# Optimization experiments

Hardware: AMD Instinct MI355X
Metric: run time of the kernel (lower is better)

The kernel has to match this reference:

```python
import jax, jax.numpy as jnp
import numpy as np
from jax import lax

B, T, D, K = 2, 4096, 128, 256


def setup_inputs() -> dict:
    key = jax.random.key(0)
    ks = jax.random.split(key, 5)
    s = 0.05
    return {
        "z": jax.random.normal(ks[0], (B, T, D), jnp.float32),
        "conv_kernel": jax.random.normal(ks[1], (K, 1, D), jnp.float32) * s,  # flax WIO depthwise
        "conv_bias": jnp.zeros((D,), jnp.float32),
        "Wq": jax.random.normal(ks[2], (D, D), jnp.float32) * s,
        "bq": jnp.zeros((D,), jnp.float32),
        "Wk": jax.random.normal(ks[3], (D, D), jnp.float32) * s,
        "bk": jnp.zeros((D,), jnp.float32),
        "Wo": jax.random.normal(ks[4], (D, D), jnp.float32) * s,
        "bo": jnp.zeros((D,), jnp.float32),
    }


def _sphere_norm(x):
    return x / jnp.maximum(jnp.linalg.norm(x, axis=-1, keepdims=True), 1e-8)


def reference(z, conv_kernel, conv_bias, Wq, bq, Wk, bk, Wo, bo):
    Bv, Tv, Dv = z.shape
    Kv = conv_kernel.shape[0]

    # Depthwise causal memory conv (flax nn.Conv, padding='CAUSAL', groups=D)
    memory_force = lax.conv_general_dilated(
        z, conv_kernel, window_strides=(1,), padding=[(Kv - 1, 0)],
        dimension_numbers=("NWC", "WIO", "NWC"), feature_group_count=Dv,
    ) + conv_bias

    # Keys are computed from the base point z once, shared across RK4 stages
    k_hat = _sphere_norm(z @ Wk + bk)  # [B,T,D]
    mask = jnp.tril(jnp.ones((Tv, Tv), z.dtype))  # causal mask

    def vector_field(z_curr):
        q_hat = _sphere_norm(z_curr @ Wq + bq)
        dots = jnp.einsum("btd,bsd->bts", q_hat, k_hat)  # [B,T,T]
        attn = jnp.sin(dots) * mask  # Kuramoto-style sin coupling, causal
        kuramoto = jnp.einsum("bts,bsd->btd", attn, k_hat) @ Wo + bo
        total = memory_force + kuramoto
        # project to tangent space of the sphere at z_curr
        return total - jnp.sum(total * z_curr, axis=-1, keepdims=True) * z_curr

    h = 1.0

    def retract(z_base, v):
        return _sphere_norm(z_base + v)

    k1 = vector_field(z)
    k2 = vector_field(retract(z, 0.5 * h * k1))
    k3 = vector_field(retract(z, 0.5 * h * k2))
    k4 = vector_field(retract(z, h * k3))
    v_final = (h / 6.0) * (k1 + 2 * k2 + 2 * k3 + k4)
    return retract(z, v_final)
```

## Files before the change

kernel.cpp:

```cpp
#include <hip/hip_runtime.h>
#include <hip/hip_bf16.h>

#define BB 2
#define TT 4096
#define DD 128
#define KK 256
#define NROW (BB*TT)
#define NELT (NROW*DD)

typedef _Float16 f16;
typedef __attribute__((ext_vector_type(8))) f16 half8;
typedef __attribute__((ext_vector_type(4))) float f32x4;

__global__ __launch_bounds__(256) void k_proj(
    const float* __restrict__ z, const float* __restrict__ Wk, const float* __restrict__ bk,
    f16* __restrict__ khb, f16* __restrict__ khT)
{
  __shared__ float Ws[DD*DD];
  __shared__ float zs[32*DD];
  int tid = threadIdx.x;
  int r0 = blockIdx.x * 32;
  #pragma unroll
  for (int it = 0; it < 16; it++){
    int idx = tid + it*256;
    *(f32x4*)(Ws + idx*4) = *(const f32x4*)(Wk + (size_t)idx*4);
  }
  #pragma unroll
  for (int it = 0; it < 4; it++){
    int idx = tid + it*256;
    *(f32x4*)(zs + idx*4) = *(const f32x4*)(z + (size_t)r0*DD + idx*4);
  }
  __syncthreads();
  int c = tid & 15, rr = tid >> 4;
  float acc0[8], acc1[8];
  #pragma unroll
  for (int u = 0; u < 8; u++){ float bv = bk[c*8+u]; acc0[u] = bv; acc1[u] = bv; }
  const float* zr0 = zs + rr*DD;
  const float* zr1 = zs + (rr+16)*DD;
  #pragma unroll 4
  for (int i = 0; i < DD; i++){
    f32x4 w0 = *(const f32x4*)(Ws + i*DD + c*8);
    f32x4 w1 = *(const f32x4*)(Ws + i*DD + c*8 + 4);
    float a0 = zr0[i], a1 = zr1[i];
    #pragma unroll
    for (int u = 0; u < 4; u++){
      acc0[u]   = fmaf(a0, w0[u], acc0[u]);   acc1[u]   = fmaf(a1, w0[u], acc1[u]);
      acc0[4+u] = fmaf(a0, w1[u], acc0[4+u]); acc1[4+u] = fmaf(a1, w1[u], acc1[4+u]);
    }
  }
  float s0 = 0.f, s1 = 0.f;
  #pragma unroll
  for (int u = 0; u < 8; u++){ s0 = fmaf(acc0[u], acc0[u], s0); s1 = fmaf(acc1[u], acc1[u], s1); }
  #pragma unroll
  for (int m = 1; m < 16; m <<= 1){ s0 += __shfl_xor(s0, m, 16); s1 += __shfl_xor(s1, m, 16); }
  float inv0 = 1.f / fmaxf(sqrtf(s0), 1e-8f);
  float inv1 = 1.f / fmaxf(sqrtf(s1), 1e-8f);
  half8 h0, h1;
  #pragma unroll
  for (int u = 0; u < 8; u++){ h0[u] = (f16)(acc0[u]*inv0); h1[u] = (f16)(acc1[u]*inv1); }
  int row0 = r0 + rr, row1 = row0 + 16;
  *(half8*)(khb + (size_t)row0*DD + c*8) = h0;
  *(half8*)(khb + (size_t)row1*DD + c*8) = h1;
  int b = row0 >> 12, t0 = row0 & 4095, t1 = row1 & 4095;
  #pragma unroll
  for (int u = 0; u < 8; u++){
    khT[((size_t)b*DD + c*8 + u)*TT + t0] = h0[u];
    khT[((size_t)b*DD + c*8 + u)*TT + t1] = h1[u];
  }
}

__global__ __launch_bounds__(256) void k_conv(
    const float* __restrict__ z, const float* __restrict__ ck, const float* __restrict__ cb,
    float* __restrict__ mf)
{
  int tid = threadIdx.x;
  int d = tid & 127, tg = tid >> 7;
  int bid = blockIdx.x;
  int b = bid >> 8;
  int tbase = ((bid & 255) << 4) + tg*8;
  const float* zb = z + (size_t)b*TT*DD;
  float acc[8];
  #pragma unroll
  for (int j = 0; j < 8; j++) acc[j] = 0.f;
  float ckq[8];
  #pragma unroll
  for (int u = 0; u < 8; u++) ckq[u] = 0.f;
  int sstart = tbase - (KK-1);
  for (int ch = 0; ch < 33; ch++){
    #pragma unroll
    for (int u = 0; u < 8; u++){
      int base = ch*8 + u;
      int s = sstart + base;
      float zv = ((unsigned)s < (unsigned)TT && base < 263) ? zb[(size_t)s*DD + d] : 0.f;
      ckq[u] = (base < KK) ? ck[(size_t)base*DD + d] : 0.f;
      #pragma unroll
      for (int j = 0; j < 8; j++) acc[j] = fmaf(ckq[(u-j)&7], zv, acc[j]);
    }
  }
  float cbv = cb[d];
  #pragma unroll
  for (int j = 0; j < 8; j++)
    mf[((size_t)b*TT + tbase + j)*DD + d] = acc[j] + cbv;
}

__global__ __launch_bounds__(256) void k_q(
    const float* __restrict__ zcur, const float* __restrict__ Wq, const float* __restrict__ bq,
    f16* __restrict__ qhb)
{
  __shared__ float Ws[DD*DD];
  __shared__ float zs[32*DD];
  int tid = threadIdx.x;
  int r0 = blockIdx.x * 32;
  #pragma unroll
  for (int it = 0; it < 16; it++){
    int idx = tid + it*256;
    *(f32x4*)(Ws + idx*4) = *(const f32x4*)(Wq + (size_t)idx*4);
  }
  #pragma unroll
  for (int it = 0; it < 4; it++){
    int idx = tid + it*256;
    *(f32x4*)(zs + idx*4) = *(const f32x4*)(zcur + (size_t)r0*DD + idx*4);
  }
  __syncthreads();
  int c = tid & 15, rr = tid >> 4;
  float acc0[8], acc1[8];
  #pragma unroll
  for (int u = 0; u < 8; u++){ float bv = bq[c*8+u]; acc0[u] = bv; acc1[u] = bv; }
  const float* zr0 = zs + rr*DD;
  const float* zr1 = zs + (rr+16)*DD;
  #pragma unroll 4
  for (int i = 0; i < DD; i++){
    f32x4 w0 = *(const f32x4*)(Ws + i*DD + c*8);
    f32x4 w1 = *(const f32x4*)(Ws + i*DD + c*8 + 4);
    float a0 = zr0[i], a1 = zr1[i];
    #pragma unroll
    for (int u = 0; u < 4; u++){
      acc0[u]   = fmaf(a0, w0[u], acc0[u]);   acc1[u]   = fmaf(a1, w0[u], acc1[u]);
      acc0[4+u] = fmaf(a0, w1[u], acc0[4+u]); acc1[4+u] = fmaf(a1, w1[u], acc1[4+u]);
    }
  }
  float s0 = 0.f, s1 = 0.f;
  #pragma unroll
  for (int u = 0; u < 8; u++){ s0 = fmaf(acc0[u], acc0[u], s0); s1 = fmaf(acc1[u], acc1[u], s1); }
  #pragma unroll
  for (int m = 1; m < 16; m <<= 1){ s0 += __shfl_xor(s0, m, 16); s1 += __shfl_xor(s1, m, 16); }
  float inv0 = 1.f / fmaxf(sqrtf(s0), 1e-8f);
  float inv1 = 1.f / fmaxf(sqrtf(s1), 1e-8f);
  half8 h0, h1;
  #pragma unroll
  for (int u = 0; u < 8; u++){ h0[u] = (f16)(acc0[u]*inv0); h1[u] = (f16)(acc1[u]*inv1); }
  *(half8*)(qhb + (size_t)(r0+rr)*DD + c*8) = h0;
  *(half8*)(qhb + (size_t)(r0+rr+16)*DD + c*8) = h1;
}

#define QTILE 128
#define NQT3 (TT/QTILE)
#define NCHUNK 272

__global__ __launch_bounds__(256,2) void k_attn4(
    const f16* __restrict__ qhb, const f16* __restrict__ khb,
    const f16* __restrict__ khT, float* __restrict__ part)
{
  int bid = blockIdx.x;
  int b = bid / NCHUNK;
  int rem = bid - b*NCHUNK;
  int qt = 0, chunk = 0;
  #pragma unroll 1
  for (int j = 0; j < NQT3; j++){
    int nch = (j + 2) >> 1;
    if (rem < nch){ qt = j; chunk = rem; break; }
    rem -= nch;
  }
  int kt0 = chunk * 4;
  int kt1 = min(kt0 + 3, 2*qt + 1);
  int t0 = qt * QTILE;

  __shared__ __align__(16) f16 Kb[64*136];
  __shared__ __align__(16) f16 Kt[128*72];
  __shared__ __align__(16) float Ps[4][32*68];

  int tid  = threadIdx.x;
  int w    = tid >> 6;
  int lane = tid & 63;
  int n16  = lane & 15;
  int g    = lane >> 4;

  const f16* qg  = qhb + (size_t)b*TT*DD;
  const f16* kg  = khb + (size_t)b*TT*DD;
  const f16* ktg = khT + (size_t)b*DD*TT;

  int sb_r  = tid >> 4, sb_c = (tid & 15)*8;
  int st_r  = tid >> 3, st_c = (tid & 7)*8;

  half8 qa[2][4];
  #pragma unroll
  for (int p = 0; p < 2; p++){
    const f16* qrow = qg + (size_t)(t0 + 32*w + 16*p + n16)*DD + g*8;
    #pragma unroll
    for (int c = 0; c < 4; c++) qa[p][c] = *(const half8*)(qrow + 32*c);
  }
  f32x4 acc[2][8];
  #pragma unroll
  for (int p = 0; p < 2; p++)
    #pragma unroll
    for (int i = 0; i < 8; i++) acc[p][i] = (f32x4){0.f,0.f,0.f,0.f};

  float* psw = &Ps[w][0];

  half8 sKb[4], sKt[4];
  {
    int s0 = kt0 * 64;
    #pragma unroll
    for (int it = 0; it < 4; it++)
      sKb[it] = *(const half8*)(kg + (size_t)(s0 + sb_r + it*16)*DD + sb_c);
    #pragma unroll
    for (int it = 0; it < 4; it++)
      sKt[it] = *(const half8*)(ktg + (size_t)(st_r + it*32)*TT + s0 + st_c);
  }

  for (int kt = kt0; kt <= kt1; kt++){
    #pragma unroll
    for (int it = 0; it < 4; it++)
      *(half8*)(Kb + (sb_r + it*16)*136 + sb_c) = sKb[it];
    #pragma unroll
    for (int it = 0; it < 4; it++)
      *(half8*)(Kt + (st_r + it*32)*72 + st_c) = sKt[it];
    __syncthreads();

    if (kt < kt1){
      int s0n = (kt+1) * 64;
      #pragma unroll
      for (int it = 0; it < 4; it++)
        sKb[it] = *(const half8*)(kg + (size_t)(s0n + sb_r + it*16)*DD + sb_c);
      #pragma unroll
      for (int it = 0; it < 4; it++)
        sKt[it] = *(const half8*)(ktg + (size_t)(st_r + it*32)*TT + s0n + st_c);
    }

    int s0 = kt * 64;
    f32x4 s_acc[2][4];
    #pragma unroll
    for (int p = 0; p < 2; p++)
      #pragma unroll
      for (int n = 0; n < 4; n++) s_acc[p][n] = (f32x4){0.f,0.f,0.f,0.f};
    #pragma unroll
    for (int c = 0; c < 4; c++){
      #pragma unroll
      for (int n = 0; n < 4; n++){
        half8 bf = *(const half8*)(Kb + (16*n + n16)*136 + 32*c + g*8);
        s_acc[0][n] = __builtin_amdgcn_mfma_f32_16x16x32_f16(qa[0][c], bf, s_acc[0][n], 0,0,0);
        s_acc[1][n] = __builtin_amdgcn_mfma_f32_16x16x32_f16(qa[1][c], bf, s_acc[1][n], 0,0,0);
      }
    }
    #pragma unroll
    for (int p = 0; p < 2; p++){
      int qrow = t0 + 32*w + 16*p + 4*g;
      #pragma unroll
      for (int n = 0; n < 4; n++){
        int key = s0 + 16*n + n16;
        #pragma unroll
        for (int r = 0; r < 4; r++){
          float v = (key <= qrow + r) ? __sinf(s_acc[p][n][r]) : 0.f;
          psw[(16*p + 4*g + r)*68 + 16*n + n16] = v;
        }
      }
    }
    __syncthreads();

    #pragma unroll
    for (int h = 0; h < 2; h++){
      half8 pa[2];
      #pragma unroll
      for (int p = 0; p < 2; p++){
        f32x4 p0 = *(const f32x4*)(psw + (16*p + n16)*68 + 32*h + 8*g);
        f32x4 p1 = *(const f32x4*)(psw + (16*p + n16)*68 + 32*h + 8*g + 4);
        pa[p][0]=(f16)p0[0]; pa[p][1]=(f16)p0[1]; pa[p][2]=(f16)p0[2]; pa[p][3]=(f16)p0[3];
        pa[p][4]=(f16)p1[0]; pa[p][5]=(f16)p1[1]; pa[p][6]=(f16)p1[2]; pa[p][7]=(f16)p1[3];
      }
      #pragma unroll
      for (int nt = 0; nt < 8; nt++){
        half8 bf = *(const half8*)(Kt + (16*nt + n16)*72 + 32*h + 8*g);
        acc[0][nt] = __builtin_amdgcn_mfma_f32_16x16x32_f16(pa[0], bf, acc[0][nt], 0,0,0);
        acc[1][nt] = __builtin_amdgcn_mfma_f32_16x16x32_f16(pa[1], bf, acc[1][nt], 0,0,0);
      }
    }
    __syncthreads();
  }

  float* pb = part + (size_t)bid*(QTILE*DD) + (32*w)*DD;
  #pragma unroll
  for (int p = 0; p < 2; p++){
    #pragma unroll
    for (int nt = 0; nt < 8; nt++){
      #pragma unroll
      for (int r = 0; r < 4; r++){
        pb[(size_t)(16*p + 4*g + r)*DD + 16*nt + n16] = acc[p][nt][r];
      }
    }
  }
}

__global__ __launch_bounds__(256) void k_reduce(
    const float* __restrict__ part, float* __restrict__ att)
{
  int bid = blockIdx.x;
  int rg = bid & 7;
  int qt = (bid >> 3) & 31;
  int b  = bid >> 8;
  int nc = (qt + 2) >> 1;
  int base = ((qt + 1)*(qt + 1)) >> 2;
  int tid = threadIdx.x;
  size_t off = (size_t)rg*(16*DD) + tid*8;
  const float* src = part + ((size_t)b*NCHUNK + base)*(QTILE*DD) + off;
  f32x4 a0 = *(const f32x4*)(src);
  f32x4 a1 = *(const f32x4*)(src + 4);
  for (int c = 1; c < nc; c++){
    const float* s2 = src + (size_t)c*(QTILE*DD);
    f32x4 b0 = *(const f32x4*)(s2);
    f32x4 b1 = *(const f32x4*)(s2 + 4);
    #pragma unroll
    for (int u = 0; u < 4; u++){ a0[u] += b0[u]; a1[u] += b1[u]; }
  }
  float* dst = att + ((size_t)b*TT + (size_t)qt*QTILE)*DD + off;
  *(f32x4*)(dst) = a0;
  *(f32x4*)(dst + 4) = a1;
}

__global__ __launch_bounds__(256) void k_comb(
    const float* __restrict__ z, const float* __restrict__ Wo, const float* __restrict__ bo,
    const float* __restrict__ mf, const float* __restrict__ att,
    const float* __restrict__ zin, float* __restrict__ zout,
    float* __restrict__ vsum, float* __restrict__ out,
    float wsum, float cretr, int first, int last)
{
  __shared__ float Ws[DD*DD];
  __shared__ float As[32*DD];
  int tid = threadIdx.x;
  int r0 = blockIdx.x * 32;
  #pragma unroll
  for (int it = 0; it < 16; it++){
    int idx = tid + it*256;
    *(f32x4*)(Ws + idx*4) = *(const f32x4*)(Wo + (size_t)idx*4);
  }
  #pragma unroll
  for (int it = 0; it < 4; it++){
    int idx = tid + it*256;
    *(f32x4*)(As + idx*4) = *(const f32x4*)(att + (size_t)r0*DD + idx*4);
  }
  __syncthreads();
  int c = tid & 15, rr = tid >> 4;
  float kur0[8], kur1[8];
  #pragma unroll
  for (int u = 0; u < 8; u++){ float bv = bo[c*8+u]; kur0[u] = bv; kur1[u] = bv; }
  const float* ar0 = As + rr*DD;
  const float* ar1 = As + (rr+16)*DD;
  #pragma unroll 4
  for (int i = 0; i < DD; i++){
    f32x4 w0 = *(const f32x4*)(Ws + i*DD + c*8);
    f32x4 w1 = *(const f32x4*)(Ws + i*DD + c*8 + 4);
    float a0 = ar0[i], a1 = ar1[i];
    #pragma unroll
    for (int u = 0; u < 4; u++){
      kur0[u]   = fmaf(a0, w0[u], kur0[u]);   kur1[u]   = fmaf(a1, w0[u], kur1[u]);
      kur0[4+u] = fmaf(a0, w1[u], kur0[4+u]); kur1[4+u] = fmaf(a1, w1[u], kur1[4+u]);
    }
  }
  size_t o0 = (size_t)(r0+rr)*DD + c*8;
  size_t o1 = (size_t)(r0+rr+16)*DD + c*8;
  float tot0[8], tot1[8], zi0[8], zi1[8];
  {
    f32x4 m0a = *(const f32x4*)(mf + o0), m0b = *(const f32x4*)(mf + o0 + 4);
    f32x4 m1a = *(const f32x4*)(mf + o1), m1b = *(const f32x4*)(mf + o1 + 4);
    f32x4 z0a = *(const f32x4*)(zin + o0), z0b = *(const f32x4*)(zin + o0 + 4);
    f32x4 z1a = *(const f32x4*)(zin + o1), z1b = *(const f32x4*)(zin + o1 + 4);
    #pragma unroll
    for (int u = 0; u < 4; u++){
      tot0[u] = m0a[u] + kur0[u]; tot0[4+u] = m0b[u] + kur0[4+u];
      tot1[u] = m1a[u] + kur1[u]; tot1[4+u] = m1b[u] + kur1[4+u];
      zi0[u] = z0a[u]; zi0[4+u] = z0b[u];
      zi1[u] = z1a[u]; zi1[4+u] = z1b[u];
    }
  }
  float p0 = 0.f, p1 = 0.f;
  #pragma unroll
  for (int u = 0; u < 8; u++){ p0 = fmaf(tot0[u], zi0[u], p0); p1 = fmaf(tot1[u], zi1[u], p1); }
  #pragma unroll
  for (int m = 1; m < 16; m <<= 1){ p0 += __shfl_xor(p0, m, 16); p1 += __shfl_xor(p1, m, 16); }
  float ki0[8], ki1[8], vs0[8], vs1[8];
  #pragma unroll
  for (int u = 0; u < 8; u++){
    ki0[u] = tot0[u] - p0 * zi0[u];
    ki1[u] = tot1[u] - p1 * zi1[u];
  }
  if (first){
    #pragma unroll
    for (int u = 0; u < 8; u++){ vs0[u] = wsum*ki0[u]; vs1[u] = wsum*ki1[u]; }
  } else {
    f32x4 v0a = *(const f32x4*)(vsum + o0), v0b = *(const f32x4*)(vsum + o0 + 4);
    f32x4 v1a = *(const f32x4*)(vsum + o1), v1b = *(const f32x4*)(vsum + o1 + 4);
    #pragma unroll
    for (int u = 0; u < 4; u++){
      vs0[u] = fmaf(wsum, ki0[u], v0a[u]); vs0[4+u] = fmaf(wsum, ki0[4+u], v0b[u]);
      vs1[u] = fmaf(wsum, ki1[u], v1a[u]); vs1[4+u] = fmaf(wsum, ki1[4+u], v1b[u]);
    }
  }
  if (!last){
    f32x4 va = {vs0[0],vs0[1],vs0[2],vs0[3]}, vb = {vs0[4],vs0[5],vs0[6],vs0[7]};
    f32x4 vc = {vs1[0],vs1[1],vs1[2],vs1[3]}, vd = {vs1[4],vs1[5],vs1[6],vs1[7]};
    *(f32x4*)(vsum + o0) = va; *(f32x4*)(vsum + o0 + 4) = vb;
    *(f32x4*)(vsum + o1) = vc; *(f32x4*)(vsum + o1 + 4) = vd;
  }
  float nz0[8], nz1[8];
  {
    f32x4 z0a = *(const f32x4*)(z + o0), z0b = *(const f32x4*)(z + o0 + 4);
    f32x4 z1a = *(const f32x4*)(z + o1), z1b = *(const f32x4*)(z + o1 + 4);
    #pragma unroll
    for (int u = 0; u < 4; u++){
      float d0a = last ? vs0[u]*(1.f/6.f)   : cretr*ki0[u];
      float d0b = last ? vs0[4+u]*(1.f/6.f) : cretr*ki0[4+u];
      float d1a = last ? vs1[u]*(1.f/6.f)   : cretr*ki1[u];
      float d1b = last ? vs1[4+u]*(1.f/6.f) : cretr*ki1[4+u];
      nz0[u] = z0a[u] + d0a; nz0[4+u] = z0b[u] + d0b;
      nz1[u] = z1a[u] + d1a; nz1[4+u] = z1b[u] + d1b;
    }
  }
  float n0 = 0.f, n1 = 0.f;
  #pragma unroll
  for (int u = 0; u < 8; u++){ n0 = fmaf(nz0[u], nz0[u], n0); n1 = fmaf(nz1[u], nz1[u], n1); }
  #pragma unroll
  for (int m = 1; m < 16; m <<= 1){ n0 += __shfl_xor(n0, m, 16); n1 += __shfl_xor(n1, m, 16); }
  float i0 = 1.f / fmaxf(sqrtf(n0), 1e-8f);
  float i1 = 1.f / fmaxf(sqrtf(n1), 1e-8f);
  float* dst = last ? out : zout;
  f32x4 ra = {nz0[0]*i0, nz0[1]*i0, nz0[2]*i0, nz0[3]*i0};
  f32x4 rb = {nz0[4]*i0, nz0[5]*i0, nz0[6]*i0, nz0[7]*i0};
  f32x4 rc = {nz1[0]*i1, nz1[1]*i1, nz1[2]*i1, nz1[3]*i1};
  f32x4 rd = {nz1[4]*i1, nz1[5]*i1, nz1[6]*i1, nz1[7]*i1};
  *(f32x4*)(dst + o0) = ra; *(f32x4*)(dst + o0 + 4) = rb;
  *(f32x4*)(dst + o1) = rc; *(f32x4*)(dst + o1 + 4) = rd;
}

extern "C" void kernel_launch(void* const* d_in, const int* in_sizes, int n_in,
                              void* d_out, int out_size, void* d_ws, size_t ws_size,
                              hipStream_t stream) {
  const float* z  = (const float*)d_in[0];
  const float* ck = (const float*)d_in[1];
  const float* cb = (const float*)d_in[2];
  const float* Wq = (const float*)d_in[3];
  const float* bq = (const float*)d_in[4];
  const float* Wk = (const float*)d_in[5];
  const float* bk = (const float*)d_in[6];
  const float* Wo = (const float*)d_in[7];
  const float* bo = (const float*)d_in[8];
  float* out = (float*)d_out;

  float* mf   = (float*)d_ws;
  float* zc   = mf   + NELT;
  float* att  = zc   + NELT;
  float* vsum = att  + NELT;
  f16*   khb  = (f16*)(vsum + NELT);
  f16*   khT  = khb  + NELT;
  f16*   qhb  = khT  + NELT;
  float* part = (float*)(qhb + NELT);

  k_proj<<<NROW/32, 256, 0, stream>>>(z, Wk, bk, khb, khT);
  k_conv<<<BB*TT/16, 256, 0, stream>>>(z, ck, cb, mf);

  const float wv[4] = {1.f, 2.f, 2.f, 1.f};
  const float cv[4] = {0.5f, 0.5f, 1.f, 0.f};
  for (int st = 0; st < 4; st++){
    const float* zcur = (st == 0) ? z : zc;
    k_q     <<<NROW/32, 256, 0, stream>>>(zcur, Wq, bq, qhb);
    k_attn4 <<<BB*NCHUNK, 256, 0, stream>>>(qhb, khb, khT, part);
    k_reduce<<<BB*NQT3*8, 256, 0, stream>>>(part, att);
    k_comb  <<<NROW/32, 256, 0, stream>>>(z, Wo, bo, mf, att, zcur, zc, vsum, out,
                                          wv[st], cv[st], st == 0, st == 3);
  }
}
```

Baseline: 316.0 us.

## Store sin scores as fp16, drop redundant barrier, fuse partial reduce into combine

The attention kernel now writes the masked sin scores into a per-wave fp16 LDS buffer instead of fp32. The P-operand load becomes one half8 read with no conversion, LDS use is smaller, and the occupancy hint goes from 2 to 3 blocks. The __syncthreads between score write and read is removed, since each wave only touches its own Ps slice. The separate k_reduce kernel is gone: k_comb sums the chunk partials directly while loading its activation tile, which saves a launch and a round-trip through the att buffer per stage, in exchange for more serial loads inside k_comb.

```diff
diff --git a/kernel.cpp b/kernel.cpp
--- a/kernel.cpp
+++ b/kernel.cpp
@@ -157,7 +157,7 @@
 #define NQT3 (TT/QTILE)
 #define NCHUNK 272
 
-__global__ __launch_bounds__(256,2) void k_attn4(
+__global__ __launch_bounds__(256,3) void k_attn5(
     const f16* __restrict__ qhb, const f16* __restrict__ khb,
     const f16* __restrict__ khT, float* __restrict__ part)
 {
@@ -177,7 +177,7 @@
 
   __shared__ __align__(16) f16 Kb[64*136];
   __shared__ __align__(16) f16 Kt[128*72];
-  __shared__ __align__(16) float Ps[4][32*68];
+  __shared__ __align__(16) f16 Ps[4][32*72];
 
   int tid  = threadIdx.x;
   int w    = tid >> 6;
@@ -205,7 +205,7 @@
     #pragma unroll
     for (int i = 0; i < 8; i++) acc[p][i] = (f32x4){0.f,0.f,0.f,0.f};
 
-  float* psw = &Ps[w][0];
+  f16* psw = &Ps[w][0];
 
   half8 sKb[4], sKt[4];
   {
@@ -261,22 +261,17 @@
         #pragma unroll
         for (int r = 0; r < 4; r++){
           float v = (key <= qrow + r) ? __sinf(s_acc[p][n][r]) : 0.f;
-          psw[(16*p + 4*g + r)*68 + 16*n + n16] = v;
+          psw[(16*p + 4*g + r)*72 + 16*n + n16] = (f16)v;
         }
       }
     }
-    __syncthreads();
 
     #pragma unroll
     for (int h = 0; h < 2; h++){
       half8 pa[2];
       #pragma unroll
-      for (int p = 0; p < 2; p++){
-        f32x4 p0 = *(const f32x4*)(psw + (16*p + n16)*68 + 32*h + 8*g);
-        f32x4 p1 = *(const f32x4*)(psw + (16*p + n16)*68 + 32*h + 8*g + 4);
-        pa[p][0]=(f16)p0[0]; pa[p][1]=(f16)p0[1]; pa[p][2]=(f16)p0[2]; pa[p][3]=(f16)p0[3];
-        pa[p][4]=(f16)p1[0]; pa[p][5]=(f16)p1[1]; pa[p][6]=(f16)p1[2]; pa[p][7]=(f16)p1[3];
-      }
+      for (int p = 0; p < 2; p++)
+        pa[p] = *(const half8*)(psw + (16*p + n16)*72 + 32*h + 8*g);
       #pragma unroll
       for (int nt = 0; nt < 8; nt++){
         half8 bf = *(const half8*)(Kt + (16*nt + n16)*72 + 32*h + 8*g);
@@ -300,35 +295,9 @@
   }
 }
 
-__global__ __launch_bounds__(256) void k_reduce(
-    const float* __restrict__ part, float* __restrict__ att)
-{
-  int bid = blockIdx.x;
-  int rg = bid & 7;
-  int qt = (bid >> 3) & 31;
-  int b  = bid >> 8;
-  int nc = (qt + 2) >> 1;
-  int base = ((qt + 1)*(qt + 1)) >> 2;
-  int tid = threadIdx.x;
-  size_t off = (size_t)rg*(16*DD) + tid*8;
-  const float* src = part + ((size_t)b*NCHUNK + base)*(QTILE*DD) + off;
-  f32x4 a0 = *(const f32x4*)(src);
-  f32x4 a1 = *(const f32x4*)(src + 4);
-  for (int c = 1; c < nc; c++){
-    const float* s2 = src + (size_t)c*(QTILE*DD);
-    f32x4 b0 = *(const f32x4*)(s2);
-    f32x4 b1 = *(const f32x4*)(s2 + 4);
-    #pragma unroll
-    for (int u = 0; u < 4; u++){ a0[u] += b0[u]; a1[u] += b1[u]; }
-  }
-  float* dst = att + ((size_t)b*TT + (size_t)qt*QTILE)*DD + off;
-  *(f32x4*)(dst) = a0;
-  *(f32x4*)(dst + 4) = a1;
-}
-
 __global__ __launch_bounds__(256) void k_comb(
     const float* __restrict__ z, const float* __restrict__ Wo, const float* __restrict__ bo,
-    const float* __restrict__ mf, const float* __restrict__ att,
+    const float* __restrict__ mf, const float* __restrict__ part,
     const float* __restrict__ zin, float* __restrict__ zout,
     float* __restrict__ vsum, float* __restrict__ out,
     float wsum, float cretr, int first, int last)
@@ -342,10 +311,25 @@
     int idx = tid + it*256;
     *(f32x4*)(Ws + idx*4) = *(const f32x4*)(Wo + (size_t)idx*4);
   }
-  #pragma unroll
-  for (int it = 0; it < 4; it++){
-    int idx = tid + it*256;
-    *(f32x4*)(As + idx*4) = *(const f32x4*)(att + (size_t)r0*DD + idx*4);
+  {
+    int b = r0 >> 12;
+    int t = r0 & 4095;
+    int qt = t >> 7;
+    int ro = t & 127;
+    int nc = (qt + 2) >> 1;
+    size_t base = ((size_t)b*NCHUNK + (((qt+1)*(qt+1)) >> 2))*(QTILE*DD) + (size_t)ro*DD;
+    #pragma unroll
+    for (int it = 0; it < 4; it++){
+      int idx = tid + it*256;
+      const float* s = part + base + idx*4;
+      f32x4 a = *(const f32x4*)(s);
+      for (int c = 1; c < nc; c++){
+        f32x4 bb = *(const f32x4*)(s + (size_t)c*(QTILE*DD));
+        #pragma unroll
+        for (int u = 0; u < 4; u++) a[u] += bb[u];
+      }
+      *(f32x4*)(As + idx*4) = a;
+    }
   }
   __syncthreads();
   int c = tid & 15, rr = tid >> 4;
@@ -456,8 +440,7 @@
 
   float* mf   = (float*)d_ws;
   float* zc   = mf   + NELT;
-  float* att  = zc   + NELT;
-  float* vsum = att  + NELT;
+  float* vsum = zc   + NELT;
   f16*   khb  = (f16*)(vsum + NELT);
   f16*   khT  = khb  + NELT;
   f16*   qhb  = khT  + NELT;
@@ -470,10 +453,9 @@
   const float cv[4] = {0.5f, 0.5f, 1.f, 0.f};
   for (int st = 0; st < 4; st++){
     const float* zcur = (st == 0) ? z : zc;
-    k_q     <<<NROW/32, 256, 0, stream>>>(zcur, Wq, bq, qhb);
-    k_attn4 <<<BB*NCHUNK, 256, 0, stream>>>(qhb, khb, khT, part);
-    k_reduce<<<BB*NQT3*8, 256, 0, stream>>>(part, att);
-    k_comb  <<<NROW/32, 256, 0, stream>>>(z, Wo, bo, mf, att, zcur, zc, vsum, out,
-                                          wv[st], cv[st], st == 0, st == 3);
-  }
-}
+    k_q    <<<NROW/32, 256, 0, stream>>>(zcur, Wq, bq, qhb);
+    k_attn5<<<BB*NCHUNK, 256, 0, stream>>>(qhb, khb, khT, part);
+    k_comb <<<NROW/32, 256, 0, stream>>>(z, Wo, bo, mf, part, zcur, zc, vsum, out,
+                                         wv[st], cv[st], st == 0, st == 3);
+  }
+}
```

New measurement: 457.5 us. 1.45x slower.
